# Kernel optimization log

Measured on AMD Instinct MI355X. Metric: run time of the kernel, lower is better.

The kernel has to match this reference:

```python
import jax, jax.numpy as jnp
import numpy as np

EPS_NORM = 1e-12  # F.normalize eps
EPS_BN = 1e-5     # BatchNorm1d eps


def _gather_neighbors(tensor, index):
    # tensor: (bs, v, d), index: (bs, v, n) -> (bs, v, n, d)
    return jax.vmap(lambda t, i: t[i])(tensor, index)


def setup_inputs() -> dict:
    key = jax.random.key(0)
    ks = jax.random.split(key, 8)
    bs, v, n = 4, 4096, 32
    cin, cout = 128, 256
    stdv = float(np.sqrt(2.0 / cout))
    return {
        "neighbor_index": jax.random.randint(ks[0], (bs, v, n), 0, v),
        "vertices": jax.random.normal(ks[1], (bs, v, 3), dtype=jnp.float32),
        "feature_map": jax.random.normal(ks[2], (bs, v, cin - 1), dtype=jnp.float32),
        "directions": jax.random.uniform(ks[3], (4, cout), minval=-stdv, maxval=stdv, dtype=jnp.float32),
        "W": jax.random.normal(ks[4], (cout, cin), dtype=jnp.float32) / np.sqrt(cin),
        "b": jnp.zeros((cout,), jnp.float32),
        "gamma": jnp.ones((cout,), jnp.float32),
        "beta": jnp.zeros((cout,), jnp.float32),
    }


def reference(neighbor_index, vertices, feature_map, directions, W, b, gamma, beta):
    # --- direction-based weights theta: (bs, v, n, cout) ---
    neighbors = _gather_neighbors(vertices, neighbor_index)          # (bs,v,n,3)
    direc = neighbors - vertices[:, :, None, :]
    direc_norm = direc / jnp.maximum(
        jnp.linalg.norm(direc, axis=-1, keepdims=True), EPS_NORM)    # F.normalize
    dir_w = (direc_norm + 1.0) * 0.5                                  # (bs,v,n,3)
    sup_w = jnp.stack([directions[1] - directions[0],
                       directions[2] - directions[0],
                       directions[3] - directions[0]], axis=0)        # (3, cout)
    theta = jax.nn.relu(jnp.einsum('bvnk,kc->bvnc', dir_w, sup_w) + directions[0])

    # --- gathered features + L2 distance channel ---
    fs = _gather_neighbors(feature_map, neighbor_index)               # (bs,v,n,cin-1)
    fdist = jnp.sqrt(jnp.sum(fs * fs, axis=-1, keepdims=True))        # (bs,v,n,1)
    fs = jnp.concatenate([fs, fdist], axis=-1)                        # (bs,v,n,cin)

    # --- Linear -> BatchNorm1d (training stats) -> ReLU ---
    z = jnp.einsum('bvni,ci->bvnc', fs, W) + b                        # (bs,v,n,cout)
    mean = jnp.mean(z, axis=(0, 1, 2))
    var = jnp.mean(jnp.square(z - mean), axis=(0, 1, 2))              # biased var
    zn = (z - mean) * jax.lax.rsqrt(var + EPS_BN) * gamma + beta
    act = jax.nn.relu(zn) * theta

    # --- max-pool over neighbor dim ---
    return jnp.max(act, axis=2)                                       # (bs,v,cout)
```

## Files before the change

### kernel.cpp

```cpp
#include <hip/hip_runtime.h>

typedef unsigned short ushort_t;
typedef __attribute__((ext_vector_type(8))) short short8;
typedef __attribute__((ext_vector_type(4))) float floatx4;
typedef __attribute__((ext_vector_type(2))) float floatx2;

#define NN    32
#define CIN   128
#define COUT  256
#define NPTS  16384
#define NSAMP (NPTS * NN)
#define LDA   136
#define HB    128

__device__ __align__(16) ushort_t g_wb[COUT * CIN];
__device__ __align__(16) ushort_t g_y[(size_t)NPTS * COUT];
__device__ __align__(16) int      g_hp[HB * 4096];
__device__ __align__(16) float    g_sp[256 * 512];
__device__ __align__(16) float    g_consts[1536];

__device__ __forceinline__ float bf2f(ushort_t u) {
    return __uint_as_float(((unsigned int)u) << 16);
}
__device__ __forceinline__ ushort_t f2bf(float f) {
    unsigned int x = __float_as_uint(f);
    return (ushort_t)((x + 0x7FFFu + ((x >> 16) & 1u)) >> 16);
}
__device__ __forceinline__ int probe_f32(const void* verts, int lane) {
    float ax = fabsf(bf2f(((const ushort_t*)verts)[lane]));
    unsigned long long b = __ballot((ax > 1e-5f) && (ax < 32.0f));
    return (__popcll(b) >= 56) ? 0 : 1;
}
__device__ __forceinline__ float bperm_f(int abytes, float v) {
    return __uint_as_float((unsigned)__builtin_amdgcn_ds_bpermute(abytes, __float_as_int(v)));
}
__device__ __forceinline__ floatx2 pk_fma(floatx2 a, floatx2 b, floatx2 c) {
    floatx2 d;
    asm("v_pk_fma_f32 %0, %1, %2, %3" : "=v"(d) : "v"(a), "v"(b), "v"(c));
    return d;
}
__device__ __forceinline__ floatx2 pk_mul(floatx2 a, floatx2 b) {
    floatx2 d;
    asm("v_pk_mul_f32 %0, %1, %2" : "=v"(d) : "v"(a), "v"(b));
    return d;
}

__global__ __launch_bounds__(256)
void hist_kernel(const int* __restrict__ nbr,
                 const void* __restrict__ Wg,
                 const void* __restrict__ verts) {
    __shared__ int h[4096];
    const int b   = blockIdx.x;
    const int tid = threadIdx.x;
    if (b < HB) {
        #pragma unroll
        for (int i = 0; i < 16; ++i) h[i * 256 + tid] = 0;
        __syncthreads();
        const int* src = nbr + (size_t)b * 4096;
        #pragma unroll
        for (int i = 0; i < 16; ++i) atomicAdd(&h[src[i * 256 + tid]], 1);
        __syncthreads();
        int* dst = g_hp + (size_t)b * 4096;
        #pragma unroll
        for (int i = 0; i < 16; ++i) dst[i * 256 + tid] = h[i * 256 + tid];
    } else {
        const int f32 = probe_f32(verts, tid & 63);
        int i = (b - HB) * 1024 + tid * 4;
        if (f32) {
            float4 v = ((const float4*)Wg)[i >> 2];
            g_wb[i] = f2bf(v.x); g_wb[i + 1] = f2bf(v.y);
            g_wb[i + 2] = f2bf(v.z); g_wb[i + 3] = f2bf(v.w);
        } else {
            *(uint2*)(g_wb + i) = *(const uint2*)((const ushort_t*)Wg + i);
        }
    }
}

__global__ __launch_bounds__(256, 2)
void ygemm_kernel(const void* __restrict__ fm, const void* __restrict__ verts) {
    __shared__ __align__(16) ushort_t At[64 * LDA];
    __shared__ float multS[64];

    const int tid  = threadIdx.x;
    const int r0   = blockIdx.x * 64;
    const int lane = tid & 63;
    const int f32  = probe_f32(verts, lane);

    if (tid < 64) {
        const int* hp = g_hp + (size_t)(r0 >> 12) * 32 * 4096 + (r0 & 4095) + tid;
        int s = 0;
        #pragma unroll
        for (int p2 = 0; p2 < 32; ++p2) s += hp[(size_t)p2 * 4096];
        multS[tid] = (float)s;
    }

    const int rl4 = tid >> 6;
    #pragma unroll 4
    for (int i = 0; i < 16; ++i) {
        const int rl = i * 4 + rl4;
        float f0, f1; ushort_t u0, u1;
        if (f32) {
            const float* src = (const float*)fm + (size_t)(r0 + rl) * 127;
            f0 = src[lane];
            f1 = (lane < 63) ? src[64 + lane] : 0.0f;
            u0 = f2bf(f0); u1 = f2bf(f1);
        } else {
            const ushort_t* src = (const ushort_t*)fm + (size_t)(r0 + rl) * 127;
            u0 = src[lane];
            u1 = (lane < 63) ? src[64 + lane] : (ushort_t)0;
            f0 = bf2f(u0); f1 = bf2f(u1);
        }
        float ss = f0 * f0 + f1 * f1;
        #pragma unroll
        for (int d = 1; d < 64; d <<= 1) ss += __shfl_xor(ss, d, 64);
        At[rl * LDA + lane]      = u0;
        At[rl * LDA + 64 + lane] = (lane < 63) ? u1 : f2bf(sqrtf(ss));
    }
    __syncthreads();

    const int w = tid >> 6;
    const int m = lane & 15;
    const int q = lane >> 4;

    floatx4 acc[4][4];
    #pragma unroll
    for (int rt = 0; rt < 4; ++rt)
        #pragma unroll
        for (int ct = 0; ct < 4; ++ct)
            acc[rt][ct] = (floatx4){0.0f, 0.0f, 0.0f, 0.0f};

    #pragma unroll
    for (int kk = 0; kk < 4; ++kk) {
        const int kof = kk * 32 + q * 8;
        short8 af[4];
        #pragma unroll
        for (int rt = 0; rt < 4; ++rt)
            af[rt] = *(const short8*)&At[(rt * 16 + m) * LDA + kof];
        short8 bfr[4];
        #pragma unroll
        for (int ct = 0; ct < 4; ++ct) {
            int ch = w * 64 + ct * 16 + m;
            bfr[ct] = *(const short8*)(g_wb + ch * CIN + kof);
        }
        #pragma unroll
        for (int rt = 0; rt < 4; ++rt)
            #pragma unroll
            for (int ct = 0; ct < 4; ++ct)
                acc[rt][ct] = __builtin_amdgcn_mfma_f32_16x16x32_bf16(
                    af[rt], bfr[ct], acc[rt][ct], 0, 0, 0);
    }

    #pragma unroll
    for (int ct = 0; ct < 4; ++ct) {
        const int ch = w * 64 + ct * 16 + m;
        float s = 0.0f, ss = 0.0f;
        #pragma unroll
        for (int rt = 0; rt < 4; ++rt)
            #pragma unroll
            for (int j = 0; j < 4; ++j) {
                int rloc = rt * 16 + q * 4 + j;
                ushort_t yb = f2bf(acc[rt][ct][j]);
                g_y[(size_t)(r0 + rloc) * COUT + ch] = yb;
                float yv = bf2f(yb);
                float wm = multS[rloc];
                s  += wm * yv;
                ss += wm * yv * yv;
            }
        s  += __shfl_xor(s, 16, 64);  s  += __shfl_xor(s, 32, 64);
        ss += __shfl_xor(ss, 16, 64); ss += __shfl_xor(ss, 32, 64);
        if (q == 0) {
            g_sp[(size_t)blockIdx.x * 512 + ch]       = s;
            g_sp[(size_t)blockIdx.x * 512 + 256 + ch] = ss;
        }
    }
}

__global__ __launch_bounds__(1024)
void finalize_kernel(const void* __restrict__ gamma,
                     const void* __restrict__ beta,
                     const void* __restrict__ dirs,
                     const void* __restrict__ verts) {
    __shared__ float redS[1024], redQ[1024];
    const int t    = threadIdx.x;
    const int c    = t & 255;
    const int part = t >> 8;
    const int f32  = probe_f32(verts, t & 63);

    float s = 0.0f, ss = 0.0f;
    #pragma unroll 8
    for (int i = 0; i < 64; ++i) {
        const int p2 = part * 64 + i;
        s  += g_sp[(size_t)p2 * 512 + c];
        ss += g_sp[(size_t)p2 * 512 + 256 + c];
    }
    redS[t] = s; redQ[t] = ss;
    __syncthreads();
    if (t < 256) {
        s  = redS[t] + redS[t + 256] + redS[t + 512] + redS[t + 768];
        ss = redQ[t] + redQ[t + 256] + redQ[t + 512] + redQ[t + 768];
        const float invN = 1.0f / (float)NSAMP;
        float mean = s * invN;
        float var  = fmaxf(ss * invN - mean * mean, 0.0f);
        float inv  = 1.0f / sqrtf(var + 1e-5f);
        float ga, be, d0, d1, d2, d3;
        if (f32) {
            ga = ((const float*)gamma)[c]; be = ((const float*)beta)[c];
            const float* dd = (const float*)dirs;
            d0 = dd[c]; d1 = dd[256 + c]; d2 = dd[512 + c]; d3 = dd[768 + c];
        } else {
            ga = bf2f(((const ushort_t*)gamma)[c]); be = bf2f(((const ushort_t*)beta)[c]);
            const ushort_t* dd = (const ushort_t*)dirs;
            d0 = bf2f(dd[c]); d1 = bf2f(dd[256 + c]);
            d2 = bf2f(dd[512 + c]); d3 = bf2f(dd[768 + c]);
        }
        float scale = ga * inv;
        g_consts[c]        = scale;
        g_consts[256 + c]  = be - mean * scale;
        g_consts[512 + c]  = d0;
        g_consts[768 + c]  = d1 - d0;
        g_consts[1024 + c] = d2 - d0;
        g_consts[1280 + c] = d3 - d0;
    }
}

__global__ __launch_bounds__(256, 4)
void epi_kernel(const int* __restrict__ nbr,
                const void* __restrict__ verts,
                void* __restrict__ out) {
    const int tid  = threadIdx.x;
    const int lane = tid & 63;
    const int bid  = blockIdx.x;
    const int p0   = (((bid & 7) << 9) | (bid >> 3)) << 2;
    const int p    = p0 + (tid >> 6);
    const int f32  = probe_f32(verts, lane);
    const int j    = lane & 31;

    int   gv;
    float wx, wy, wz;
    {
        gv = ((p >> 12) << 12) + nbr[(size_t)p * NN + j];
        float sx, sy, sz, nx, ny, nz;
        if (f32) {
            const float* vv = (const float*)verts;
            sx = vv[p * 3]; sy = vv[p * 3 + 1]; sz = vv[p * 3 + 2];
            nx = vv[gv * 3]; ny = vv[gv * 3 + 1]; nz = vv[gv * 3 + 2];
        } else {
            const ushort_t* vv = (const ushort_t*)verts;
            sx = bf2f(vv[p * 3]); sy = bf2f(vv[p * 3 + 1]); sz = bf2f(vv[p * 3 + 2]);
            nx = bf2f(vv[gv * 3]); ny = bf2f(vv[gv * 3 + 1]); nz = bf2f(vv[gv * 3 + 2]);
        }
        float dx = nx - sx, dy = ny - sy, dz = nz - sz;
        float nrm = sqrtf(dx * dx + dy * dy + dz * dz);
        float inv = 1.0f / fmaxf(nrm, 1e-12f);
        wx = (dx * inv + 1.0f) * 0.5f;
        wy = (dy * inv + 1.0f) * 0.5f;
        wz = (dz * inv + 1.0f) * 0.5f;
    }

    const int hsel = (lane >> 5) << 2;
    const int cofs = (lane & 31) << 4;
    const int c8   = (lane & 31) * 8;

    const floatx2 zero2 = {0.0f, 0.0f};
    floatx2 sc2[4], sh2[4], d02[4], s02[4], s12[4], s22[4];
    #pragma unroll
    for (int c = 0; c < 4; ++c) {
        sc2[c] = *(const floatx2*)&g_consts[c8 + 2 * c];
        sh2[c] = *(const floatx2*)&g_consts[256 + c8 + 2 * c];
        d02[c] = *(const floatx2*)&g_consts[512 + c8 + 2 * c];
        s02[c] = *(const floatx2*)&g_consts[768 + c8 + 2 * c];
        s12[c] = *(const floatx2*)&g_consts[1024 + c8 + 2 * c];
        s22[c] = *(const floatx2*)&g_consts[1280 + c8 + 2 * c];
    }

    const char* gyb = (const char*)g_y;
    floatx2 acc2[4] = {zero2, zero2, zero2, zero2};
    uint4 u[4]; floatx2 bxp[4], byp[4], bzp[4];

    #pragma unroll
    for (int k = 0; k < 4; ++k) {
        const int av = k * 8 + hsel;
        int rw = __builtin_amdgcn_ds_bpermute(av, gv);
        float t0 = bperm_f(av, wx), t1 = bperm_f(av, wy), t2 = bperm_f(av, wz);
        bxp[k] = (floatx2){t0, t0};
        byp[k] = (floatx2){t1, t1};
        bzp[k] = (floatx2){t2, t2};
        u[k] = *(const uint4*)(gyb + (((unsigned)rw << 9) + (unsigned)cofs));
    }
    #pragma unroll
    for (int g = 0; g < 4; ++g) {
        #pragma unroll
        for (int k = 0; k < 4; ++k) {
            const uint4 uk = u[k];
            const floatx2 wxk = bxp[k], wyk = byp[k], wzk = bzp[k];
            if (g < 3) {
                const int av = (g * 4 + k + 4) * 8 + hsel;
                int rw = __builtin_amdgcn_ds_bpermute(av, gv);
                float t0 = bperm_f(av, wx), t1 = bperm_f(av, wy), t2 = bperm_f(av, wz);
                bxp[k] = (floatx2){t0, t0};
                byp[k] = (floatx2){t1, t1};
                bzp[k] = (floatx2){t2, t2};
                u[k] = *(const uint4*)(gyb + (((unsigned)rw << 9) + (unsigned)cofs));
            }
            const unsigned uc[4] = {uk.x, uk.y, uk.z, uk.w};
            #pragma unroll
            for (int c = 0; c < 4; ++c) {
                floatx2 y;
                y.x = __uint_as_float(uc[c] << 16);
                y.y = __uint_as_float(uc[c] & 0xFFFF0000u);
                floatx2 th = pk_fma(wzk, s22[c],
                             pk_fma(wyk, s12[c],
                             pk_fma(wxk, s02[c], d02[c])));
                th = __builtin_elementwise_max(th, zero2);
                floatx2 zt = pk_mul(pk_fma(y, sc2[c], sh2[c]), th);
                acc2[c] = __builtin_elementwise_max(acc2[c], zt);
            }
        }
    }

    #pragma unroll
    for (int c = 0; c < 4; ++c) {
        acc2[c].x = fmaxf(acc2[c].x, __shfl_xor(acc2[c].x, 32, 64));
        acc2[c].y = fmaxf(acc2[c].y, __shfl_xor(acc2[c].y, 32, 64));
    }

    if (lane < 32) {
        size_t ofs = (size_t)p * COUT + c8;
        if (f32) {
            floatx4 oL = {acc2[0].x, acc2[0].y, acc2[1].x, acc2[1].y};
            floatx4 oH = {acc2[2].x, acc2[2].y, acc2[3].x, acc2[3].y};
            *(floatx4*)((float*)out + ofs)     = oL;
            *(floatx4*)((float*)out + ofs + 4) = oH;
        } else {
            uint4 ou;
            ou.x = ((unsigned int)f2bf(acc2[0].y) << 16) | (unsigned int)f2bf(acc2[0].x);
            ou.y = ((unsigned int)f2bf(acc2[1].y) << 16) | (unsigned int)f2bf(acc2[1].x);
            ou.z = ((unsigned int)f2bf(acc2[2].y) << 16) | (unsigned int)f2bf(acc2[2].x);
            ou.w = ((unsigned int)f2bf(acc2[3].y) << 16) | (unsigned int)f2bf(acc2[3].x);
            *(uint4*)((ushort_t*)out + ofs) = ou;
        }
    }
}

extern "C" void kernel_launch(void* const* d_in, const int* in_sizes, int n_in,
                              void* d_out, int out_size, void* d_ws, size_t ws_size,
                              hipStream_t stream) {
    const int* nbr    = (const int*)d_in[0];
    const void* verts = d_in[1];
    const void* fm    = d_in[2];
    const void* dirs  = d_in[3];
    const void* Wg    = d_in[4];
    const void* gamma = d_in[6];
    const void* beta  = d_in[7];
    (void)d_ws; (void)ws_size; (void)in_sizes; (void)n_in; (void)out_size;

    hist_kernel<<<dim3(HB + 32), dim3(256), 0, stream>>>(nbr, Wg, verts);
    ygemm_kernel<<<dim3(NPTS / 64), dim3(256), 0, stream>>>(fm, verts);
    finalize_kernel<<<dim3(1), dim3(1024), 0, stream>>>(gamma, beta, dirs, verts);
    epi_kernel<<<dim3(NPTS / 4), dim3(256), 0, stream>>>(nbr, verts, d_out);
}
```

Measured before the change: 139.2 us.

## Fuse BN finalize into GEMM via last-block counter and precompute feature norms

Removes the separate single-block finalize kernel by having the last ygemm block, detected with an atomic counter, reduce the partial statistics and write the BN and direction constants. The per-row feature L2 norm moves into extra blocks of the histogram kernel, so the GEMM no longer does a 64-lane shuffle reduction per row. GEMM tiles shrink from 64 to 32 rows, doubling the block count to 512 for more parallelism. The cost is a serial 512-partial reduction done by one block at the tail of the GEMM, plus a global counter that must be reset for every call.

```diff
diff --git a/kernel.cpp b/kernel.cpp
--- a/kernel.cpp
+++ b/kernel.cpp
@@ -12,12 +12,15 @@
 #define NSAMP (NPTS * NN)
 #define LDA   136
 #define HB    128
+#define YGB   512
 
 __device__ __align__(16) ushort_t g_wb[COUT * CIN];
 __device__ __align__(16) ushort_t g_y[(size_t)NPTS * COUT];
 __device__ __align__(16) int      g_hp[HB * 4096];
-__device__ __align__(16) float    g_sp[256 * 512];
+__device__ __align__(16) float    g_fd[NPTS];
+__device__ __align__(16) float    g_sp[YGB * 512];
 __device__ __align__(16) float    g_consts[1536];
+__device__            int         g_ctr;
 
 __device__ __forceinline__ float bf2f(ushort_t u) {
     return __uint_as_float(((unsigned int)u) << 16);
@@ -48,6 +51,7 @@
 __global__ __launch_bounds__(256)
 void hist_kernel(const int* __restrict__ nbr,
                  const void* __restrict__ Wg,
+                 const void* __restrict__ fm,
                  const void* __restrict__ verts) {
     __shared__ int h[4096];
     const int b   = blockIdx.x;
@@ -63,7 +67,7 @@
         int* dst = g_hp + (size_t)b * 4096;
         #pragma unroll
         for (int i = 0; i < 16; ++i) dst[i * 256 + tid] = h[i * 256 + tid];
-    } else {
+    } else if (b < HB + 32) {
         const int f32 = probe_f32(verts, tid & 63);
         int i = (b - HB) * 1024 + tid * 4;
         if (f32) {
@@ -73,20 +77,43 @@
         } else {
             *(uint2*)(g_wb + i) = *(const uint2*)((const ushort_t*)Wg + i);
         }
+    } else {
+        const int f32 = probe_f32(verts, tid & 63);
+        const int row = (b - HB - 32) * 64 + (tid >> 2);
+        const int q   = tid & 3;
+        const int n   = 32 - (q == 3);
+        float ss = 0.0f;
+        if (f32) {
+            const float* src = (const float*)fm + (size_t)row * 127 + q * 32;
+            #pragma unroll 8
+            for (int i = 0; i < 32; ++i)
+                if (i < n) { float v = src[i]; ss += v * v; }
+        } else {
+            const ushort_t* src = (const ushort_t*)fm + (size_t)row * 127 + q * 32;
+            #pragma unroll 8
+            for (int i = 0; i < 32; ++i)
+                if (i < n) { float v = bf2f(src[i]); ss += v * v; }
+        }
+        ss += __shfl_xor(ss, 1, 64);
+        ss += __shfl_xor(ss, 2, 64);
+        if (q == 0) g_fd[row] = sqrtf(ss);
     }
 }
 
 __global__ __launch_bounds__(256, 2)
-void ygemm_kernel(const void* __restrict__ fm, const void* __restrict__ verts) {
-    __shared__ __align__(16) ushort_t At[64 * LDA];
-    __shared__ float multS[64];
+void ygemm_kernel(const void* __restrict__ fm, const void* __restrict__ verts,
+                  const void* __restrict__ gamma, const void* __restrict__ beta,
+                  const void* __restrict__ dirs) {
+    __shared__ __align__(16) ushort_t At[32 * LDA];
+    __shared__ float multS[32];
+    __shared__ int lastB;
 
     const int tid  = threadIdx.x;
-    const int r0   = blockIdx.x * 64;
+    const int r0   = blockIdx.x * 32;
     const int lane = tid & 63;
     const int f32  = probe_f32(verts, lane);
 
-    if (tid < 64) {
+    if (tid < 32) {
         const int* hp = g_hp + (size_t)(r0 >> 12) * 32 * 4096 + (r0 & 4095) + tid;
         int s = 0;
         #pragma unroll
@@ -95,26 +122,21 @@
     }
 
     const int rl4 = tid >> 6;
-    #pragma unroll 4
-    for (int i = 0; i < 16; ++i) {
+    #pragma unroll
+    for (int i = 0; i < 8; ++i) {
         const int rl = i * 4 + rl4;
-        float f0, f1; ushort_t u0, u1;
+        ushort_t u0, u1;
         if (f32) {
             const float* src = (const float*)fm + (size_t)(r0 + rl) * 127;
-            f0 = src[lane];
-            f1 = (lane < 63) ? src[64 + lane] : 0.0f;
-            u0 = f2bf(f0); u1 = f2bf(f1);
+            u0 = f2bf(src[lane]);
+            u1 = (lane < 63) ? f2bf(src[64 + lane]) : (ushort_t)0;
         } else {
             const ushort_t* src = (const ushort_t*)fm + (size_t)(r0 + rl) * 127;
             u0 = src[lane];
             u1 = (lane < 63) ? src[64 + lane] : (ushort_t)0;
-            f0 = bf2f(u0); f1 = bf2f(u1);
-        }
-        float ss = f0 * f0 + f1 * f1;
-        #pragma unroll
-        for (int d = 1; d < 64; d <<= 1) ss += __shfl_xor(ss, d, 64);
+        }
         At[rl * LDA + lane]      = u0;
-        At[rl * LDA + 64 + lane] = (lane < 63) ? u1 : f2bf(sqrtf(ss));
+        At[rl * LDA + 64 + lane] = (lane < 63) ? u1 : f2bf(g_fd[r0 + rl]);
     }
     __syncthreads();
 
@@ -122,9 +144,9 @@
     const int m = lane & 15;
     const int q = lane >> 4;
 
-    floatx4 acc[4][4];
-    #pragma unroll
-    for (int rt = 0; rt < 4; ++rt)
+    floatx4 acc[2][4];
+    #pragma unroll
+    for (int rt = 0; rt < 2; ++rt)
         #pragma unroll
         for (int ct = 0; ct < 4; ++ct)
             acc[rt][ct] = (floatx4){0.0f, 0.0f, 0.0f, 0.0f};
@@ -132,9 +154,9 @@
     #pragma unroll
     for (int kk = 0; kk < 4; ++kk) {
         const int kof = kk * 32 + q * 8;
-        short8 af[4];
-        #pragma unroll
-        for (int rt = 0; rt < 4; ++rt)
+        short8 af[2];
+        #pragma unroll
+        for (int rt = 0; rt < 2; ++rt)
             af[rt] = *(const short8*)&At[(rt * 16 + m) * LDA + kof];
         short8 bfr[4];
         #pragma unroll
@@ -143,7 +165,7 @@
             bfr[ct] = *(const short8*)(g_wb + ch * CIN + kof);
         }
         #pragma unroll
-        for (int rt = 0; rt < 4; ++rt)
+        for (int rt = 0; rt < 2; ++rt)
             #pragma unroll
             for (int ct = 0; ct < 4; ++ct)
                 acc[rt][ct] = __builtin_amdgcn_mfma_f32_16x16x32_bf16(
@@ -155,7 +177,7 @@
         const int ch = w * 64 + ct * 16 + m;
         float s = 0.0f, ss = 0.0f;
         #pragma unroll
-        for (int rt = 0; rt < 4; ++rt)
+        for (int rt = 0; rt < 2; ++rt)
             #pragma unroll
             for (int j = 0; j < 4; ++j) {
                 int rloc = rt * 16 + q * 4 + j;
@@ -173,54 +195,42 @@
             g_sp[(size_t)blockIdx.x * 512 + 256 + ch] = ss;
         }
     }
-}
-
-__global__ __launch_bounds__(1024)
-void finalize_kernel(const void* __restrict__ gamma,
-                     const void* __restrict__ beta,
-                     const void* __restrict__ dirs,
-                     const void* __restrict__ verts) {
-    __shared__ float redS[1024], redQ[1024];
-    const int t    = threadIdx.x;
-    const int c    = t & 255;
-    const int part = t >> 8;
-    const int f32  = probe_f32(verts, t & 63);
-
+
+    __threadfence();
+    if (tid == 0) lastB = (atomicAdd(&g_ctr, 1) == YGB - 1) ? 1 : 0;
+    __syncthreads();
+    if (!lastB) return;
+    if (tid == 0) g_ctr = 0;
+    __threadfence();
+    const int c = tid;
     float s = 0.0f, ss = 0.0f;
     #pragma unroll 8
-    for (int i = 0; i < 64; ++i) {
-        const int p2 = part * 64 + i;
+    for (int p2 = 0; p2 < YGB; ++p2) {
         s  += g_sp[(size_t)p2 * 512 + c];
         ss += g_sp[(size_t)p2 * 512 + 256 + c];
     }
-    redS[t] = s; redQ[t] = ss;
-    __syncthreads();
-    if (t < 256) {
-        s  = redS[t] + redS[t + 256] + redS[t + 512] + redS[t + 768];
-        ss = redQ[t] + redQ[t + 256] + redQ[t + 512] + redQ[t + 768];
-        const float invN = 1.0f / (float)NSAMP;
-        float mean = s * invN;
-        float var  = fmaxf(ss * invN - mean * mean, 0.0f);
-        float inv  = 1.0f / sqrtf(var + 1e-5f);
-        float ga, be, d0, d1, d2, d3;
-        if (f32) {
-            ga = ((const float*)gamma)[c]; be = ((const float*)beta)[c];
-            const float* dd = (const float*)dirs;
-            d0 = dd[c]; d1 = dd[256 + c]; d2 = dd[512 + c]; d3 = dd[768 + c];
-        } else {
-            ga = bf2f(((const ushort_t*)gamma)[c]); be = bf2f(((const ushort_t*)beta)[c]);
-            const ushort_t* dd = (const ushort_t*)dirs;
-            d0 = bf2f(dd[c]); d1 = bf2f(dd[256 + c]);
-            d2 = bf2f(dd[512 + c]); d3 = bf2f(dd[768 + c]);
-        }
-        float scale = ga * inv;
-        g_consts[c]        = scale;
-        g_consts[256 + c]  = be - mean * scale;
-        g_consts[512 + c]  = d0;
-        g_consts[768 + c]  = d1 - d0;
-        g_consts[1024 + c] = d2 - d0;
-        g_consts[1280 + c] = d3 - d0;
-    }
+    const float invN = 1.0f / (float)NSAMP;
+    float mean = s * invN;
+    float var  = fmaxf(ss * invN - mean * mean, 0.0f);
+    float inv  = 1.0f / sqrtf(var + 1e-5f);
+    float ga, be, d0, d1, d2, d3;
+    if (f32) {
+        ga = ((const float*)gamma)[c]; be = ((const float*)beta)[c];
+        const float* dd = (const float*)dirs;
+        d0 = dd[c]; d1 = dd[256 + c]; d2 = dd[512 + c]; d3 = dd[768 + c];
+    } else {
+        ga = bf2f(((const ushort_t*)gamma)[c]); be = bf2f(((const ushort_t*)beta)[c]);
+        const ushort_t* dd = (const ushort_t*)dirs;
+        d0 = bf2f(dd[c]); d1 = bf2f(dd[256 + c]);
+        d2 = bf2f(dd[512 + c]); d3 = bf2f(dd[768 + c]);
+    }
+    float scale = ga * inv;
+    g_consts[c]        = scale;
+    g_consts[256 + c]  = be - mean * scale;
+    g_consts[512 + c]  = d0;
+    g_consts[768 + c]  = d1 - d0;
+    g_consts[1024 + c] = d2 - d0;
+    g_consts[1280 + c] = d3 - d0;
 }
 
 __global__ __launch_bounds__(256, 4)
@@ -354,8 +364,7 @@
     const void* beta  = d_in[7];
     (void)d_ws; (void)ws_size; (void)in_sizes; (void)n_in; (void)out_size;
 
-    hist_kernel<<<dim3(HB + 32), dim3(256), 0, stream>>>(nbr, Wg, verts);
-    ygemm_kernel<<<dim3(NPTS / 64), dim3(256), 0, stream>>>(fm, verts);
-    finalize_kernel<<<dim3(1), dim3(1024), 0, stream>>>(gamma, beta, dirs, verts);
+    hist_kernel<<<dim3(HB + 32 + 256), dim3(256), 0, stream>>>(nbr, Wg, fm, verts);
+    ygemm_kernel<<<dim3(YGB), dim3(256), 0, stream>>>(fm, verts, gamma, beta, dirs);
     epi_kernel<<<dim3(NPTS / 4), dim3(256), 0, stream>>>(nbr, verts, d_out);
 }
```

Result: slower. 231.8 us (+66.6%).
